# Kernel optimization log

Hardware: AMD Instinct MI355X
Metric: run time of the kernel (lower is better)

The kernel has to match this reference:

```python
import jax, jax.numpy as jnp
import numpy as np

T, A, E, RAW, H, NACT, NTP = 64, 48, 22, 512, 256, 21, 3
# entity_distinct: self entity [0], friendly entities [1:12], hostile entities [12:22]
PARAM_SHAPES = [
    ("W1", (NTP, RAW, H)), ("b1", (NTP, H)), ("W2", (NTP, H, H)), ("b2", (NTP, H)),
    ("WCf", (NTP, 2 * H, H)), ("bCf", (NTP, H)), ("WMf", (NTP, 2 * H + 2 * RAW, H)), ("bMf", (NTP, H)),
    ("WCh", (NTP, 2 * H, H)), ("bCh", (NTP, H)), ("WMh", (NTP, 2 * H + 2 * RAW, H)), ("bMh", (NTP, H)),
    ("L1", (NTP, 2 * H, H)), ("bL1", (NTP, H)), ("L2", (NTP, H, H // 2)), ("bL2", (NTP, H // 2)),
    ("L3", (NTP, H // 2, NACT)), ("bL3", (NTP, NACT)),
    ("V1", (NTP, 2 * H, H)), ("bV1", (NTP, H)), ("V2", (NTP, H, 1)), ("bV2", (NTP, 1)),
]
PNAMES = [n for n, _ in PARAM_SHAPES]


def setup_inputs() -> dict:
    key = jax.random.key(0)
    ks = jax.random.split(key, 3 + len(PARAM_SHAPES))
    inp = {
        "obs": jax.random.normal(ks[0], (T, A, E, RAW), jnp.float32),
        "hete_pick": jax.random.randint(ks[1], (T, A), 0, NTP, jnp.int32),
        "dead": jax.random.bernoulli(ks[2], 0.15, (T, A, E)),
    }
    for i, (n, s) in enumerate(PARAM_SHAPES):
        inp[n] = jax.random.normal(ks[3 + i], s, jnp.float32) * 0.02
    return inp


def _net_forward(p, obs, dead):
    relu = jax.nn.relu
    obs = jnp.where(dead[..., None], 0.0, obs)                    # nan_to_num for dead entities
    v = relu(obs @ p["W1"] + p["b1"]) @ p["W2"] + p["b2"]         # [T,A,E,H] per-entity encoder
    zs, ze_f, ze_h = obs[..., 0, :], obs[..., 1:12, :], obs[..., 12:22, :]
    vs, ve_f, ve_h = v[..., 0, :], v[..., 1:12, :], v[..., 12:22, :]
    df, dh = dead[..., 1:12], dead[..., 12:22]

    def conc(ve, d, ze, WC, bC, WM, bM):
        w = (~d).astype(obs.dtype)                                # alive mask [T,A,Ef]
        denom = jnp.maximum(w.sum(-1, keepdims=True), 1.0)
        pool = jnp.einsum('taeh,tae->tah', ve, w) / denom         # masked mean over entities
        pool_z = jnp.einsum('taer,tae->tar', ze, w) / denom       # skip-connect raw-obs pool
        vC = relu(jnp.concatenate([vs, pool], -1) @ WC + bC)
        vM = relu(jnp.concatenate([vs, pool, zs, pool_z], -1) @ WM + bM)
        return vC, vM

    vfC, vfM = conc(ve_f, df, ze_f, p["WCf"], p["bCf"], p["WMf"], p["bMf"])
    vhC, vhM = conc(ve_h, dh, ze_h, p["WCh"], p["bCh"], p["WMh"], p["bMh"])
    vC = jnp.concatenate([vfC, vhC], -1)                          # [T,A,2H] dual-conc fuse
    vM = jnp.concatenate([vfM, vhM], -1)
    logits = relu(relu(vC @ p["L1"] + p["bL1"]) @ p["L2"] + p["bL2"]) @ p["L3"] + p["bL3"]
    value = relu(vM @ p["V1"] + p["bV1"]) @ p["V2"] + p["bV2"]    # [T,A,1]
    logp = jax.nn.log_softmax(logits, -1)
    act = jnp.argmax(logits, -1)                                  # deterministic (test_mode) action
    alp = jnp.take_along_axis(logp, act[..., None], -1)           # [T,A,1] action log-prob
    return act, value, alp


def reference(obs, hete_pick, dead, W1, b1, W2, b2, WCf, bCf, WMf, bMf, WCh, bCh, WMh, bMh,
              L1, bL1, L2, bL2, L3, bL3, V1, bV1, V2, bV2):
    params = dict(W1=W1, b1=b1, W2=W2, b2=b2, WCf=WCf, bCf=bCf, WMf=WMf, bMf=bMf,
                  WCh=WCh, bCh=bCh, WMh=WMh, bMh=bMh, L1=L1, bL1=bL1, L2=L2, bL2=bL2,
                  L3=L3, bL3=bL3, V1=V1, bV1=bV1, V2=V2, bV2=bV2)
    act = jnp.zeros((T, A), jnp.int32)
    value = jnp.zeros((T, A, 1), obs.dtype)
    alp = jnp.zeros((T, A, 1), obs.dtype)
    for t in range(NTP):                                          # heterogeneous dispatch (distribute_compute)
        pt = {k: v[t] for k, v in params.items()}
        a_t, v_t, lp_t = _net_forward(pt, obs, dead)
        m = hete_pick == t                                        # mask_arr[t]
        act = jnp.where(m, a_t.astype(jnp.int32), act)
        value = jnp.where(m[..., None], v_t, value)
        alp = jnp.where(m[..., None], lp_t, alp)
    return act, value, alp
```

## Files before the change

kernel.cpp:

```cpp
#include <hip/hip_runtime.h>
#include <cstdint>

#define T_ 64
#define A_ 48
#define NP_ 3072
#define E_ 22
#define RAW_ 512
#define H_ 256
#define NACT_ 21
#define NTP_ 3
#define PV_ 3456
#define RV_ 68096
#define NDEAD_ 67584

typedef unsigned short u16;
typedef __attribute__((ext_vector_type(8))) short short8;
typedef __attribute__((ext_vector_type(4))) short short4v;
typedef __attribute__((ext_vector_type(4))) float floatx4;

__device__ __forceinline__ u16 f2bf(float x) {
    unsigned r;
    asm("v_cvt_pk_bf16_f32 %0, %1, %1" : "=v"(r) : "v"(x));
    return (u16)r;
}
__device__ __forceinline__ float bf2f(u16 h) {
    return __uint_as_float(((unsigned)h) << 16);
}

typedef __attribute__((address_space(1))) const void* gp_t;
typedef __attribute__((address_space(3))) void* lp_t;
__device__ __forceinline__ void gload16(const void* g, void* l) {
    __builtin_amdgcn_global_load_lds((gp_t)g, (lp_t)l, 16, 0, 0);
}

__device__ __forceinline__ void sync_tile() {
    asm volatile("s_waitcnt vmcnt(0) lgkmcnt(0)" ::: "memory");
    __builtin_amdgcn_s_barrier();
    __builtin_amdgcn_sched_barrier(0);
}

__device__ __forceinline__ int swzk(int r) { return ((r >> 1) ^ r) & 3; }

__global__ void k_bucket(const unsigned* __restrict__ deadRaw,
                         const int* __restrict__ hete, int* __restrict__ wsI)
{
    __shared__ int fl[2];
    __shared__ int sc[3], cur[3], sps[3], srs[3];
    int tid = threadIdx.x;
    if (tid < 2) fl[tid] = 0;
    if (tid < 3) { sc[tid] = 0; cur[tid] = 0; }
    __syncthreads();
    int ni = 0, nf = 0;
    for (int i = tid; i < 1024; i += 256) {
        unsigned w = deadRaw[i];
        if (w > 1u) ni = 1;
        if (w != 0u && w != 0x3F800000u) nf = 1;
    }
    if (ni) atomicOr(&fl[0], 1);
    if (nf) atomicOr(&fl[1], 1);
    for (int p = tid; p < NP_; p += 256) atomicAdd(&sc[hete[p]], 1);
    __syncthreads();
    if (tid == 0) {
        int c0 = sc[0], c1 = sc[1], c2 = sc[2];
        int p1 = (c0 + 127) & ~127;
        int p2 = p1 + ((c1 + 127) & ~127);
        sps[0] = 0; sps[1] = p1; sps[2] = p2;
        int r1 = (22 * c0 + 127) & ~127;
        int r2 = r1 + ((22 * c1 + 127) & ~127);
        srs[0] = 0; srs[1] = r1; srs[2] = r2;
        wsI[0] = fl[0] ? (fl[1] ? 2 : 1) : 0;
        wsI[1] = c0; wsI[2] = c1; wsI[3] = c2;
        wsI[4] = 0; wsI[5] = p1; wsI[6] = p2;
        wsI[8] = 0; wsI[9] = r1; wsI[10] = r2;
    }
    __syncthreads();
    int* pairIdx = wsI + 16;
    int* prb = pairIdx + PV_;
    for (int pv = tid; pv < PV_; pv += 256) pairIdx[pv] = -1;
    __syncthreads();
    for (int p = tid; p < NP_; p += 256) {
        int t = hete[p];
        int pos = atomicAdd(&cur[t], 1);
        pairIdx[sps[t] + pos] = p;
    }
    for (int pv = tid; pv < PV_; pv += 256) {
        int t = (pv >= sps[1]) + (pv >= sps[2]);
        prb[pv] = srs[t] + 22 * (pv - sps[t]);
    }
}

__global__ void k_deadmask(const void* __restrict__ dead,
                           const int* __restrict__ wsI, float* __restrict__ dm)
{
    int i = blockIdx.x * 256 + threadIdx.x;
    if (i >= NDEAD_) return;
    int mode = wsI[0];
    bool d;
    if (mode == 0)      d = ((const int*)dead)[i] != 0;
    else if (mode == 1) d = ((const float*)dead)[i] != 0.f;
    else                d = ((const unsigned char*)dead)[i] != 0;
    dm[i] = d ? 0.f : 1.f;
}

__global__ void k_rowobs(const int* __restrict__ cnt, const int* __restrict__ ps,
                         const int* __restrict__ rs, const int* __restrict__ pairIdx,
                         const float* __restrict__ dm, int* __restrict__ rowObs)
{
    int rv = blockIdx.x * 256 + threadIdx.x;
    if (rv >= RV_) return;
    int t = (rv >= rs[1]) + (rv >= rs[2]);
    int local = rv - rs[t];
    int out = -1;
    if (local < 22 * cnt[t]) {
        int pl = local / 22;
        int e = local - pl * 22;
        int p = pairIdx[ps[t] + pl];
        if (p >= 0) {
            int oi = p * 22 + e;
            if (dm[oi] != 0.f) out = oi;
        }
    }
    rowObs[rv] = out;
}

struct WCA {
    const float* W[8]; u16* Hi[8]; u16* Lo[8]; int K[8]; int bs[9];
};
__global__ __launch_bounds__(256) void k_wconv(WCA a)
{
    int blk = blockIdx.x;
    int s = 0;
#pragma unroll
    for (int i = 1; i < 8; ++i) if (blk >= a.bs[i]) s = i;
    int lb = blk - a.bs[s];
    int K = a.K[s];
    int K8 = K >> 3;
    int kc = lb % K8;
    int t  = lb / K8;
    int n  = threadIdx.x;
    const float* w = a.W[s] + (long)t * K * 256 + n;
    short8 hv, lv;
#pragma unroll
    for (int j = 0; j < 8; ++j) {
        float x = w[(long)(kc * 8 + j) * 256];
        u16 hh = f2bf(x);
        hv[j] = (short)hh;
        lv[j] = (short)f2bf(x - bf2f(hh));
    }
    long o = ((long)t * 256 + n) * K + kc * 8;
    *(short8*)(a.Hi[s] + o) = hv;
    *(short8*)(a.Lo[s] + o) = lv;
}

struct GD {
    const void* Aa; const void* Ab;
    const u16* Bh; const u16* Bl;
    const float* bias;
    void* Ca; void* Cb;
    long lda; long ldc;
    int K; int coff;
};
struct GA4 { GD d[4]; };

template<int AMODE, bool RELU, int OUTS>
__global__ __launch_bounds__(256) void k_mgemm(
    GA4 ga, const int* __restrict__ rowIdx, const int* __restrict__ starts)
{
    __shared__ short smem[32768];
    const int tid = threadIdx.x;
    const GD d = ga.d[blockIdx.z];
    const long rb = (long)blockIdx.x * 128;
    const int n0 = blockIdx.y * 128;
    const int t = (rb >= starts[0]) + (rb >= starts[1]);
    const int K = d.K;
    const long lda = d.lda;
    const u16* bhT = d.Bh + ((long)t * 256 + n0) * K;
    const u16* blT = d.Bl + ((long)t * 256 + n0) * K;
    const float* biasT = d.bias + (long)t * 256 + n0;

    const int cs = tid & 3;

    const int ar = tid >> 3;
    const int ac = (tid & 7) * 4;
    long arow[4]; float amask[4];
    const float* Afp = (const float*)d.Aa;
    if (AMODE == 1) {
#pragma unroll
        for (int it = 0; it < 4; ++it) {
            int r = 32 * it + ar;
            int i0 = rowIdx[rb + r];
            amask[it] = (i0 < 0) ? 0.f : 1.f;
            arow[it] = (i0 < 0) ? 0 : (long)i0 * lda;
        }
    }
    const u16* ahT = (const u16*)d.Aa;
    const u16* alT = (const u16*)d.Ab;

    const int wave = tid >> 6;
    const int lane = tid & 63;
    const int wr = (wave >> 1) * 64;
    const int wc = (wave & 1) * 64;
    const int lm = lane & 15;
    const int quad = lane >> 4;

    auto stageB = [&](int b, int k0) {
        short* Bh = smem + b * 16384 + 8192;
        short* Bl = smem + b * 16384 + 12288;
#pragma unroll
        for (int i = 0; i < 2; ++i) {
            int c = i * 256 + tid;
            int r = c >> 2;
            long go = (long)r * K + k0 + ((cs ^ swzk(r)) << 3);
            gload16(bhT + go, &Bh[c << 3]);
            gload16(blT + go, &Bl[c << 3]);
        }
    };
    auto stageA0 = [&](int b, int k0) {
        short* Ah = smem + b * 16384;
        short* Al = smem + b * 16384 + 4096;
#pragma unroll
        for (int i = 0; i < 2; ++i) {
            int c = i * 256 + tid;
            int r = c >> 2;
            long go = (rb + r) * lda + k0 + ((cs ^ swzk(r)) << 3);
            gload16(ahT + go, &Ah[c << 3]);
            gload16(alT + go, &Al[c << 3]);
        }
    };
    auto convertA = [&](int b, const float4* av) {
        short* AhW = smem + b * 16384;
        short* AlW = AhW + 4096;
#pragma unroll
        for (int it = 0; it < 4; ++it) {
            float xs[4] = {av[it].x, av[it].y, av[it].z, av[it].w};
            short4v hv, lv;
#pragma unroll
            for (int e = 0; e < 4; ++e) {
                float x = xs[e] * amask[it];
                u16 hh = f2bf(x);
                hv[e] = (short)hh;
                lv[e] = (short)f2bf(x - bf2f(hh));
            }
            int r = 32 * it + ar;
            int bs = (((ac >> 3) ^ swzk(r)) << 4) | ((ac & 4) << 1);
            *(short4v*)((char*)AhW + r * 64 + bs) = hv;
            *(short4v*)((char*)AlW + r * 64 + bs) = lv;
        }
    };

    floatx4 acc[4][4];
#pragma unroll
    for (int i = 0; i < 4; ++i)
#pragma unroll
        for (int j = 0; j < 4; ++j) acc[i][j] = (floatx4){0.f, 0.f, 0.f, 0.f};

    if (AMODE == 1) {
        float4 av0[4];
#pragma unroll
        for (int it = 0; it < 4; ++it)
            av0[it] = *(const float4*)(Afp + arow[it] + ac);
        stageB(0, 0);
        convertA(0, av0);
    } else {
        stageA0(0, 0);
        stageB(0, 0);
    }
    sync_tile();

    const int nt = K >> 5;
    int cur = 0;
    for (int ti = 0; ti < nt; ++ti) {
        const bool pf = (ti + 1) < nt;
        const int k1 = (ti + 1) << 5;
        float4 av2[4];
        if (pf) {
            if (AMODE == 1) {
#pragma unroll
                for (int it = 0; it < 4; ++it)
                    av2[it] = *(const float4*)(Afp + arow[it] + k1 + ac);
            } else {
                stageA0(cur ^ 1, k1);
            }
            stageB(cur ^ 1, k1);
        }
        const short* Ah = smem + cur * 16384;
        const short* Al = Ah + 4096;
        const short* Bh = Ah + 8192;
        const short* Bl = Ah + 12288;
        short8 fah[4], fal[4];
#pragma unroll
        for (int i = 0; i < 4; ++i) {
            int m = wr + 16 * i + lm;
            int sl = (quad ^ swzk(m)) << 3;
            fah[i] = *(const short8*)&Ah[(m << 5) + sl];
            fal[i] = *(const short8*)&Al[(m << 5) + sl];
        }
#pragma unroll
        for (int j = 0; j < 4; ++j) {
            int n = wc + 16 * j + lm;
            int sl = (quad ^ swzk(n)) << 3;
            short8 fbh = *(const short8*)&Bh[(n << 5) + sl];
            short8 fbl = *(const short8*)&Bl[(n << 5) + sl];
#pragma unroll
            for (int i = 0; i < 4; ++i) {
                acc[i][j] = __builtin_amdgcn_mfma_f32_16x16x32_bf16(fah[i], fbh, acc[i][j], 0, 0, 0);
                acc[i][j] = __builtin_amdgcn_mfma_f32_16x16x32_bf16(fal[i], fbh, acc[i][j], 0, 0, 0);
                acc[i][j] = __builtin_amdgcn_mfma_f32_16x16x32_bf16(fah[i], fbl, acc[i][j], 0, 0, 0);
            }
        }
        if (pf && AMODE == 1) convertA(cur ^ 1, av2);
        sync_tile();
        cur ^= 1;
    }

    if (OUTS == 0) {
        float* C = (float*)d.Ca;
#pragma unroll
        for (int j = 0; j < 4; ++j) {
            int col = wc + 16 * j + lm;
            float bj = biasT[col];
#pragma unroll
            for (int i = 0; i < 4; ++i) {
                long rbase = rb + wr + 16 * i + quad * 4;
#pragma unroll
                for (int r = 0; r < 4; ++r) {
                    float vv = acc[i][j][r] + bj;
                    if (RELU) vv = fmaxf(vv, 0.f);
                    C[(rbase + r) * d.ldc + d.coff + n0 + col] = vv;
                }
            }
        }
    } else {
        u16* Chi = (u16*)smem;
        u16* Clo = Chi + 16384;
#pragma unroll
        for (int j = 0; j < 4; ++j) {
            int col = wc + 16 * j + lm;
            float bj = biasT[col];
#pragma unroll
            for (int i = 0; i < 4; ++i) {
                int row0 = wr + 16 * i + quad * 4;
#pragma unroll
                for (int r = 0; r < 4; ++r) {
                    float vv = acc[i][j][r] + bj;
                    if (RELU) vv = fmaxf(vv, 0.f);
                    int row = row0 + r;
                    int cc = col ^ (((row >> 2) & 3) << 4);
                    u16 hh = f2bf(vv);
                    Chi[row * 128 + cc] = hh;
                    Clo[row * 128 + cc] = f2bf(vv - bf2f(hh));
                }
            }
        }
        asm volatile("s_waitcnt lgkmcnt(0)" ::: "memory");
        __builtin_amdgcn_s_barrier();
        __builtin_amdgcn_sched_barrier(0);
        u16* Ca = (u16*)d.Ca;
        u16* Cb = (u16*)d.Cb;
#pragma unroll
        for (int s = 0; s < 8; ++s) {
            int ch = s * 256 + tid;
            int row = ch >> 4;
            int gcol = (ch & 15) * 8;
            int lo = row * 128 + (gcol ^ (((row >> 2) & 3) << 4));
            short8 hv = *(const short8*)&Chi[lo];
            short8 lv = *(const short8*)&Clo[lo];
            long go = (rb + row) * d.ldc + d.coff + n0 + gcol;
            *(short8*)(Ca + go) = hv;
            *(short8*)(Cb + go) = lv;
        }
    }
}

__global__ __launch_bounds__(256) void k_prep(
    const int* __restrict__ pairIdx, const int* __restrict__ prb,
    const float* __restrict__ dm, const float* __restrict__ v,
    const float* __restrict__ obs,
    u16* __restrict__ XFh, u16* __restrict__ XFl,
    u16* __restrict__ XHh, u16* __restrict__ XHl)
{
    int pv = blockIdx.x, c = threadIdx.x;
    int p = pairIdx[pv];
    long xo = (long)pv * 1536;
    if (p < 0) {
        for (int s = 0; s < 6; ++s) {
            XFh[xo + s * 256 + c] = 0; XFl[xo + s * 256 + c] = 0;
            XHh[xo + s * 256 + c] = 0; XHl[xo + s * 256 + c] = 0;
        }
        return;
    }
    __shared__ float sw[22];
    if (c < 22) sw[c] = dm[p * 22 + c];
    __syncthreads();
    float denf = 0.f, denh = 0.f;
    for (int e = 1; e < 12; ++e)  denf += sw[e];
    for (int e = 12; e < 22; ++e) denh += sw[e];
    denf = 1.f / fmaxf(denf, 1.f);
    denh = 1.f / fmaxf(denh, 1.f);

    auto wsp = [&](u16* Hh, u16* Hl, long idx, float val) {
        u16 hh = f2bf(val);
        Hh[idx] = hh;
        Hl[idx] = f2bf(val - bf2f(hh));
    };

    long base = prb[pv];
    float vs = v[base * 256 + c];
    wsp(XFh, XFl, xo + c, vs);
    wsp(XHh, XHl, xo + c, vs);
    float af = 0.f, ah = 0.f;
    for (int e = 1; e < 12; ++e)  af += sw[e] * v[(base + e) * 256 + c];
    for (int e = 12; e < 22; ++e) ah += sw[e] * v[(base + e) * 256 + c];
    wsp(XFh, XFl, xo + 256 + c, af * denf);
    wsp(XHh, XHl, xo + 256 + c, ah * denh);
    const float* ob = obs + (long)p * 22 * 512;
    float w0 = sw[0];
    float z0 = ob[c] * w0;
    float z1 = ob[256 + c] * w0;
    wsp(XFh, XFl, xo + 512 + c, z0); wsp(XHh, XHl, xo + 512 + c, z0);
    wsp(XFh, XFl, xo + 768 + c, z1); wsp(XHh, XHl, xo + 768 + c, z1);
#pragma unroll
    for (int half = 0; half < 2; ++half) {
        int c2 = c + half * 256;
        float zf = 0.f, zh = 0.f;
        for (int e = 1; e < 12; ++e)  zf += sw[e] * ob[(long)e * 512 + c2];
        for (int e = 12; e < 22; ++e) zh += sw[e] * ob[(long)e * 512 + c2];
        wsp(XFh, XFl, xo + 1024 + c2, zf * denf);
        wsp(XHh, XHl, xo + 1024 + c2, zh * denh);
    }
}

__global__ __launch_bounds__(128) void k_final(
    const float* __restrict__ g1, const float* __restrict__ vV,
    const float* __restrict__ L2, const float* __restrict__ bL2,
    const float* __restrict__ L3, const float* __restrict__ bL3,
    const float* __restrict__ V2, const float* __restrict__ bV2,
    const int* __restrict__ pairIdx, const int* __restrict__ ps,
    float* __restrict__ out)
{
    int pv = blockIdx.x;
    int p = pairIdx[pv];
    if (p < 0) return;
    int c = threadIdx.x;
    int t = (pv >= ps[1]) + (pv >= ps[2]);

    __shared__ float sg1[256], sg2[128], sval[2];
    const float* g1p = g1 + (long)pv * 256;
    sg1[c] = g1p[c];
    sg1[c + 128] = g1p[c + 128];

    const float* vv = vV + (long)pv * 256;
    const float* v2t = V2 + t * 256;
    float s = vv[c] * v2t[c] + vv[c + 128] * v2t[c + 128];
    for (int off = 32; off; off >>= 1) s += __shfl_down(s, off);
    if ((c & 63) == 0) sval[c >> 6] = s;
    __syncthreads();

    const float* l2 = L2 + (long)t * 256 * 128 + c;
    float a = bL2[t * 128 + c];
#pragma unroll 8
    for (int k = 0; k < 256; ++k) a = fmaf(sg1[k], l2[(long)k * 128], a);
    sg2[c] = fmaxf(a, 0.f);
    __syncthreads();

    if (c < 64) {
        float lg = -3.0e38f;
        if (c < 21) {
            const float* l3t = L3 + (long)t * 128 * 21 + c;
            float acc = bL3[t * 21 + c];
            for (int k = 0; k < 128; ++k) acc = fmaf(sg2[k], l3t[k * 21], acc);
            lg = acc;
        }
        float mv = lg; int mi = (c < 21) ? c : 9999;
        for (int off = 32; off; off >>= 1) {
            float ov = __shfl_down(mv, off);
            int oi = __shfl_down(mi, off);
            if (ov > mv || (ov == mv && oi < mi)) { mv = ov; mi = oi; }
        }
        mv = __shfl(mv, 0); mi = __shfl(mi, 0);
        float e = (c < 21) ? expf(lg - mv) : 0.f;
        for (int off = 32; off; off >>= 1) e += __shfl_down(e, off);
        if (c == 0) {
            out[p] = (float)mi;
            out[NP_ + p] = sval[0] + sval[1] + bV2[t];
            out[2 * NP_ + p] = -logf(e);
        }
    }
}

extern "C" void kernel_launch(void* const* d_in, const int* in_sizes, int n_in,
                              void* d_out, int out_size, void* d_ws, size_t ws_size,
                              hipStream_t stream)
{
    const float* obs = (const float*)d_in[0];
    const int* hete = (const int*)d_in[1];
    const void* dead = d_in[2];
    const float* W1 = (const float*)d_in[3];  const float* b1 = (const float*)d_in[4];
    const float* W2 = (const float*)d_in[5];  const float* b2 = (const float*)d_in[6];
    const float* WCf = (const float*)d_in[7]; const float* bCf = (const float*)d_in[8];
    const float* WMf = (const float*)d_in[9]; const float* bMf = (const float*)d_in[10];
    const float* WCh = (const float*)d_in[11]; const float* bCh = (const float*)d_in[12];
    const float* WMh = (const float*)d_in[13]; const float* bMh = (const float*)d_in[14];
    const float* L1 = (const float*)d_in[15]; const float* bL1 = (const float*)d_in[16];
    const float* L2 = (const float*)d_in[17]; const float* bL2 = (const float*)d_in[18];
    const float* L3 = (const float*)d_in[19]; const float* bL3 = (const float*)d_in[20];
    const float* V1 = (const float*)d_in[21]; const float* bV1 = (const float*)d_in[22];
    const float* V2 = (const float*)d_in[23]; const float* bV2 = (const float*)d_in[24];
    float* out = (float*)d_out;

    int* wsI = (int*)d_ws;
    int* pairIdx = wsI + 16;
    int* prb = pairIdx + PV_;
    int* rowObs = prb + PV_;
    long fbase = ((16L + PV_ + PV_ + RV_) + 63) & ~63L;
    float* wsF = (float*)d_ws;
    float* dm = wsF + fbase;
    float* cur = dm + NDEAD_;
    auto allocUS = [&](long K) { u16* p = (u16*)cur; cur += (3L * 256 * K) / 2; return p; };
    u16* W1h = allocUS(512);  u16* W1l = allocUS(512);
    u16* W2h = allocUS(256);  u16* W2l = allocUS(256);
    u16* WCfh = allocUS(512); u16* WCfl = allocUS(512);
    u16* WChh = allocUS(512); u16* WChl = allocUS(512);
    u16* WMfh = allocUS(1536); u16* WMfl = allocUS(1536);
    u16* WMhh = allocUS(1536); u16* WMhl = allocUS(1536);
    u16* L1h = allocUS(512);  u16* L1l = allocUS(512);
    u16* V1h = allocUS(512);  u16* V1l = allocUS(512);
    float* regA = cur;
    float* regB = regA + (long)RV_ * 256;

    u16* h1h = (u16*)regA;
    u16* h1l = h1h + (long)RV_ * 256;
    u16* XFh = (u16*)regA;
    u16* XFl = XFh + (long)PV_ * 1536;
    u16* XHh = XFl + (long)PV_ * 1536;
    u16* XHl = XHh + (long)PV_ * 1536;
    float* v = regB;
    u16* vCh = (u16*)regB;
    u16* vCl = vCh + (long)PV_ * 512;
    u16* vMh = vCl + (long)PV_ * 512;
    u16* vMl = vMh + (long)PV_ * 512;
    float* g1 = (float*)(vMl + (long)PV_ * 512);
    float* vV = g1 + (long)PV_ * 256;

    k_bucket<<<1, 256, 0, stream>>>((const unsigned*)dead, hete, wsI);
    k_deadmask<<<264, 256, 0, stream>>>(dead, wsI, dm);
    k_rowobs<<<266, 256, 0, stream>>>(wsI + 1, wsI + 4, wsI + 8, pairIdx, dm, rowObs);

    {
        WCA wa;
        const float* Ws[8] = {W1, W2, WCf, WCh, WMf, WMh, L1, V1};
        u16* His[8] = {W1h, W2h, WCfh, WChh, WMfh, WMhh, L1h, V1h};
        u16* Los[8] = {W1l, W2l, WCfl, WChl, WMfl, WMhl, L1l, V1l};
        int Ks[8] = {512, 256, 512, 512, 1536, 1536, 512, 512};
        int acc_b = 0; wa.bs[0] = 0;
        for (int i = 0; i < 8; ++i) {
            wa.W[i] = Ws[i]; wa.Hi[i] = His[i]; wa.Lo[i] = Los[i]; wa.K[i] = Ks[i];
            acc_b += 3 * Ks[i] / 8; wa.bs[i + 1] = acc_b;
        }
        k_wconv<<<acc_b, 256, 0, stream>>>(wa);
    }

    GA4 g;
    auto setd = [&](int i, const void* Aa, const void* Ab, const u16* Bh_, const u16* Bl_,
                    const float* bias, void* Ca, void* Cb, long lda_, long ldc_, int K_, int coff_) {
        g.d[i] = GD{Aa, Ab, Bh_, Bl_, bias, Ca, Cb, lda_, ldc_, K_, coff_};
    };

    for (int i = 0; i < 4; ++i)
        setd(i, obs, nullptr, W1h, W1l, b1, h1h, h1l, 512, 256, 512, 0);
    k_mgemm<1, true, 1><<<dim3(RV_ / 128, 2, 1), 256, 0, stream>>>(g, rowObs, wsI + 9);

    for (int i = 0; i < 4; ++i)
        setd(i, h1h, h1l, W2h, W2l, b2, v, nullptr, 256, 256, 256, 0);
    k_mgemm<0, false, 0><<<dim3(RV_ / 128, 2, 1), 256, 0, stream>>>(g, nullptr, wsI + 9);

    k_prep<<<PV_, 256, 0, stream>>>(pairIdx, prb, dm, v, obs, XFh, XFl, XHh, XHl);

    setd(0, XFh, XFl, WCfh, WCfl, bCf, vCh, vCl, 1536, 512, 512, 0);
    setd(1, XHh, XHl, WChh, WChl, bCh, vCh, vCl, 1536, 512, 512, 256);
    setd(2, XFh, XFl, WMfh, WMfl, bMf, vMh, vMl, 1536, 512, 1536, 0);
    setd(3, XHh, XHl, WMhh, WMhl, bMh, vMh, vMl, 1536, 512, 1536, 256);
    k_mgemm<0, true, 1><<<dim3(PV_ / 128, 2, 4), 256, 0, stream>>>(g, nullptr, wsI + 5);

    setd(0, vCh, vCl, L1h, L1l, bL1, g1, nullptr, 512, 256, 512, 0);
    setd(1, vMh, vMl, V1h, V1l, bV1, vV, nullptr, 512, 256, 512, 0);
    setd(2, vCh, vCl, L1h, L1l, bL1, g1, nullptr, 512, 256, 512, 0);
    setd(3, vCh, vCl, L1h, L1l, bL1, g1, nullptr, 512, 256, 512, 0);
    k_mgemm<0, true, 0><<<dim3(PV_ / 128, 2, 2), 256, 0, stream>>>(g, nullptr, wsI + 5);

    k_final<<<PV_, 128, 0, stream>>>(g1, vV, L2, bL2, L3, bL3, V2, bV2,
                                     pairIdx, wsI + 4, out);
    (void)in_sizes; (void)n_in; (void)out_size; (void)ws_size;
}
```

Measured before the change: 520.3 us.

## Restructure GEMM main loop into register-prefetched, two-stage unrolled software pipeline

Rewrites the k_mgemm main loop so A tiles are loaded into registers with inline-asm global loads two K-steps ahead, and B tiles go through async LDS loads one step ahead. Explicit vmcnt waits let memory traffic overlap the MFMA block instead of draining everything at each tile barrier. It also raises MFMA wave priority during compute and adds a min-2-blocks occupancy hint. The hand-counted vmcnt values and the clamped tail K indices (which redundantly reload the last tile) must be exactly right, which adds correctness risk and register pressure.

```diff
diff --git a/kernel.cpp b/kernel.cpp
--- a/kernel.cpp
+++ b/kernel.cpp
@@ -33,10 +33,27 @@
     __builtin_amdgcn_global_load_lds((gp_t)g, (lp_t)l, 16, 0, 0);
 }
 
-__device__ __forceinline__ void sync_tile() {
-    asm volatile("s_waitcnt vmcnt(0) lgkmcnt(0)" ::: "memory");
-    __builtin_amdgcn_s_barrier();
-    __builtin_amdgcn_sched_barrier(0);
+__device__ __forceinline__ floatx4 ld_f4(const float* p) {
+    floatx4 r;
+    asm volatile("global_load_dwordx4 %0, %1, off" : "=&v"(r) : "v"(p));
+    return r;
+}
+__device__ __forceinline__ short8 ld_s8(const u16* p) {
+    short8 r;
+    asm volatile("global_load_dwordx4 %0, %1, off" : "=&v"(r) : "v"(p));
+    return r;
+}
+template<int N>
+__device__ __forceinline__ void wait_vm_f(floatx4 (&a)[4]) {
+    asm volatile("s_waitcnt vmcnt(%4)"
+                 : "+v"(a[0]), "+v"(a[1]), "+v"(a[2]), "+v"(a[3])
+                 : "i"(N) : "memory");
+}
+template<int N>
+__device__ __forceinline__ void wait_vm_s(short8 (&a)[4]) {
+    asm volatile("s_waitcnt vmcnt(%4)"
+                 : "+v"(a[0]), "+v"(a[1]), "+v"(a[2]), "+v"(a[3])
+                 : "i"(N) : "memory");
 }
 
 __device__ __forceinline__ int swzk(int r) { return ((r >> 1) ^ r) & 3; }
@@ -163,7 +180,7 @@
 struct GA4 { GD d[4]; };
 
 template<int AMODE, bool RELU, int OUTS>
-__global__ __launch_bounds__(256) void k_mgemm(
+__global__ __launch_bounds__(256, 2) void k_mgemm(
     GA4 ga, const int* __restrict__ rowIdx, const int* __restrict__ starts)
 {
     __shared__ short smem[32768];
@@ -179,6 +196,8 @@
     const float* biasT = d.bias + (long)t * 256 + n0;
 
     const int cs = tid & 3;
+    const int r0 = tid >> 2;
+    const int r1 = 64 + r0;
 
     const int ar = tid >> 3;
     const int ac = (tid & 7) * 4;
@@ -203,7 +222,7 @@
     const int lm = lane & 15;
     const int quad = lane >> 4;
 
-    auto stageB = [&](int b, int k0) {
+    auto issueB = [&](int b, int k0) {
         short* Bh = smem + b * 16384 + 8192;
         short* Bl = smem + b * 16384 + 12288;
 #pragma unroll
@@ -215,28 +234,26 @@
             gload16(blT + go, &Bl[c << 3]);
         }
     };
-    auto stageA0 = [&](int b, int k0) {
-        short* Ah = smem + b * 16384;
-        short* Al = smem + b * 16384 + 4096;
-#pragma unroll
-        for (int i = 0; i < 2; ++i) {
-            int c = i * 256 + tid;
-            int r = c >> 2;
-            long go = (rb + r) * lda + k0 + ((cs ^ swzk(r)) << 3);
-            gload16(ahT + go, &Ah[c << 3]);
-            gload16(alT + go, &Al[c << 3]);
-        }
-    };
-    auto convertA = [&](int b, const float4* av) {
+    auto issueA1 = [&](int k0, floatx4 (&dst)[4]) {
+#pragma unroll
+        for (int it = 0; it < 4; ++it)
+            dst[it] = ld_f4(Afp + arow[it] + k0 + ac);
+    };
+    auto issueA0 = [&](int k0, short8 (&dst)[4]) {
+        dst[0] = ld_s8(ahT + (rb + r0) * lda + k0 + cs * 8);
+        dst[1] = ld_s8(ahT + (rb + r1) * lda + k0 + cs * 8);
+        dst[2] = ld_s8(alT + (rb + r0) * lda + k0 + cs * 8);
+        dst[3] = ld_s8(alT + (rb + r1) * lda + k0 + cs * 8);
+    };
+    auto writeA1 = [&](int b, floatx4 (&src)[4]) {
         short* AhW = smem + b * 16384;
         short* AlW = AhW + 4096;
 #pragma unroll
         for (int it = 0; it < 4; ++it) {
-            float xs[4] = {av[it].x, av[it].y, av[it].z, av[it].w};
             short4v hv, lv;
 #pragma unroll
             for (int e = 0; e < 4; ++e) {
-                float x = xs[e] * amask[it];
+                float x = src[it][e] * amask[it];
                 u16 hh = f2bf(x);
                 hv[e] = (short)hh;
                 lv[e] = (short)f2bf(x - bf2f(hh));
@@ -247,6 +264,14 @@
             *(short4v*)((char*)AlW + r * 64 + bs) = lv;
         }
     };
+    auto writeA0 = [&](int b, short8 (&src)[4]) {
+        short* AhW = smem + b * 16384;
+        short* AlW = AhW + 4096;
+        *(short8*)((char*)AhW + r0 * 64 + ((cs ^ swzk(r0)) << 4)) = src[0];
+        *(short8*)((char*)AhW + r1 * 64 + ((cs ^ swzk(r1)) << 4)) = src[1];
+        *(short8*)((char*)AlW + r0 * 64 + ((cs ^ swzk(r0)) << 4)) = src[2];
+        *(short8*)((char*)AlW + r1 * 64 + ((cs ^ swzk(r1)) << 4)) = src[3];
+    };
 
     floatx4 acc[4][4];
 #pragma unroll
@@ -254,36 +279,8 @@
 #pragma unroll
         for (int j = 0; j < 4; ++j) acc[i][j] = (floatx4){0.f, 0.f, 0.f, 0.f};
 
-    if (AMODE == 1) {
-        float4 av0[4];
-#pragma unroll
-        for (int it = 0; it < 4; ++it)
-            av0[it] = *(const float4*)(Afp + arow[it] + ac);
-        stageB(0, 0);
-        convertA(0, av0);
-    } else {
-        stageA0(0, 0);
-        stageB(0, 0);
-    }
-    sync_tile();
-
-    const int nt = K >> 5;
-    int cur = 0;
-    for (int ti = 0; ti < nt; ++ti) {
-        const bool pf = (ti + 1) < nt;
-        const int k1 = (ti + 1) << 5;
-        float4 av2[4];
-        if (pf) {
-            if (AMODE == 1) {
-#pragma unroll
-                for (int it = 0; it < 4; ++it)
-                    av2[it] = *(const float4*)(Afp + arow[it] + k1 + ac);
-            } else {
-                stageA0(cur ^ 1, k1);
-            }
-            stageB(cur ^ 1, k1);
-        }
-        const short* Ah = smem + cur * 16384;
+    auto computeT = [&](int b) {
+        const short* Ah = smem + b * 16384;
         const short* Al = Ah + 4096;
         const short* Bh = Ah + 8192;
         const short* Bl = Ah + 12288;
@@ -295,6 +292,7 @@
             fah[i] = *(const short8*)&Ah[(m << 5) + sl];
             fal[i] = *(const short8*)&Al[(m << 5) + sl];
         }
+        __builtin_amdgcn_s_setprio(1);
 #pragma unroll
         for (int j = 0; j < 4; ++j) {
             int n = wc + 16 * j + lm;
@@ -308,10 +306,51 @@
                 acc[i][j] = __builtin_amdgcn_mfma_f32_16x16x32_bf16(fah[i], fbl, acc[i][j], 0, 0, 0);
             }
         }
-        if (pf && AMODE == 1) convertA(cur ^ 1, av2);
-        sync_tile();
-        cur ^= 1;
-    }
+        __builtin_amdgcn_s_setprio(0);
+    };
+
+    floatx4 fS0[4], fS1[4];
+    short8  s0[4], s1[4];
+    const int nt = K >> 5;
+
+    if (AMODE == 1) issueA1(0, fS0); else issueA0(0, s0);
+    issueB(0, 0);
+    if (AMODE == 1) { wait_vm_f<4>(fS0); writeA1(0, fS0); }
+    else            { wait_vm_s<4>(s0);  writeA0(0, s0); }
+    if (AMODE == 1) issueA1(32, fS1); else issueA0(32, s1);
+    asm volatile("s_waitcnt vmcnt(4) lgkmcnt(0)" ::: "memory");
+    __builtin_amdgcn_s_barrier();
+    __builtin_amdgcn_sched_barrier(0);
+
+    for (int ti = 0; ti < nt; ti += 2) {
+        {
+            const int kB = ((ti + 1 < nt) ? ti + 1 : nt - 1) << 5;
+            const int kA = ((ti + 2 < nt) ? ti + 2 : nt - 1) << 5;
+            issueB(1, kB);
+            if (AMODE == 1) issueA1(kA, fS0); else issueA0(kA, s0);
+            computeT(0);
+            if (AMODE == 1) { wait_vm_f<8>(fS1); writeA1(1, fS1); }
+            else            { wait_vm_s<8>(s1);  writeA0(1, s1); }
+            asm volatile("s_waitcnt vmcnt(4) lgkmcnt(0)" ::: "memory");
+            __builtin_amdgcn_s_barrier();
+            __builtin_amdgcn_sched_barrier(0);
+        }
+        {
+            const int kB = ((ti + 2 < nt) ? ti + 2 : nt - 1) << 5;
+            const int kA = ((ti + 3 < nt) ? ti + 3 : nt - 1) << 5;
+            issueB(0, kB);
+            if (AMODE == 1) issueA1(kA, fS1); else issueA0(kA, s1);
+            computeT(1);
+            if (AMODE == 1) { wait_vm_f<8>(fS0); writeA1(0, fS0); }
+            else            { wait_vm_s<8>(s0);  writeA0(0, s0); }
+            asm volatile("s_waitcnt vmcnt(4) lgkmcnt(0)" ::: "memory");
+            __builtin_amdgcn_s_barrier();
+            __builtin_amdgcn_sched_barrier(0);
+        }
+    }
+    asm volatile("s_waitcnt vmcnt(0) lgkmcnt(0)" ::: "memory");
+    __builtin_amdgcn_s_barrier();
+    __builtin_amdgcn_sched_barrier(0);
 
     if (OUTS == 0) {
         float* C = (float*)d.Ca;
```

After: 505.7 us. 2.8% less time.
